# Optimization experiments

Hardware: AMD Instinct MI355X
Metric: run time of the kernel (lower is better)

## Reference

```python
import jax, jax.numpy as jnp
import numpy as np

B, N, C = 16, 1024, 768
NUM_HEADS = 8
HEAD_DIM = C // NUM_HEADS
TEMP_INIT = 0.05
EPS_NORM = 1e-12   # F.normalize eps
EPS_LN = 1e-5      # LayerNorm eps


def setup_inputs() -> dict:
    key = jax.random.key(0)
    ks = jax.random.split(key, 4)
    x = jax.random.normal(ks[0], (B, N, C), dtype=jnp.float32)
    w_qkv = jax.random.normal(ks[1], (3 * C, C), dtype=jnp.float32) * (1.0 / np.sqrt(C))
    w_proj = jax.random.normal(ks[2], (C, C), dtype=jnp.float32) * (1.0 / np.sqrt(C))
    temperature = jnp.ones((NUM_HEADS, 1, 1), dtype=jnp.float32) * TEMP_INIT
    conv_w = jax.random.normal(ks[3], (C, 1, 3, 3), dtype=jnp.float32) * (1.0 / 3.0)
    gamma = jnp.ones((C,), dtype=jnp.float32)
    beta = jnp.zeros((C,), dtype=jnp.float32)
    return {"x": x, "w_qkv": w_qkv, "w_proj": w_proj, "temperature": temperature,
            "conv_w": conv_w, "gamma": gamma, "beta": beta, "H": 32, "W": 32}


def _l2norm_tokens(t):
    # normalize along token dim (axis=-2), matching F.normalize(dim=-2)
    n = jnp.sqrt(jnp.sum(t * t, axis=-2, keepdims=True))
    return t / jnp.maximum(n, EPS_NORM)


def reference(x, w_qkv, w_proj, temperature, conv_w, gamma, beta, H, W):
    b, n, c = x.shape
    h, d = NUM_HEADS, HEAD_DIM
    qkv = (x @ w_qkv.T).reshape(b, n, 3, h, d).transpose(2, 0, 3, 1, 4)  # [3,B,h,N,d]
    q, k, v = qkv[0], qkv[1], qkv[2]
    q = _l2norm_tokens(q)
    k = _l2norm_tokens(k)
    # cross-covariance attention over channels: [B,h,d,d]
    A = jnp.einsum('bhnd,bhne->bhde', q, k) / temperature[None]
    A = jax.nn.softmax(A, axis=-1)
    # v @ A^T : [B,h,N,d]
    x_xca = jnp.einsum('bhne,bhde->bhnd', v, A)
    x_xca = x_xca.transpose(0, 2, 1, 3).reshape(b, n, c)
    x_xca = x_xca @ w_proj.T
    # depthwise 3x3 local propagation
    x_img = x.transpose(0, 2, 1).reshape(b, c, H, W)
    x_local = jax.lax.conv_general_dilated(
        x_img, conv_w, window_strides=(1, 1), padding=((1, 1), (1, 1)),
        dimension_numbers=('NCHW', 'OIHW', 'NCHW'), feature_group_count=c)
    x_local = x_local.reshape(b, c, n).transpose(0, 2, 1)
    y = x_xca + 0.1 * x_local
    mu = jnp.mean(y, axis=-1, keepdims=True)
    var = jnp.mean((y - mu) ** 2, axis=-1, keepdims=True)
    return (y - mu) * jax.lax.rsqrt(var + EPS_LN) * gamma + beta
```

## Files before the change

kernel.cpp:

```cpp
#include <hip/hip_runtime.h>

#define DEVI __device__ __forceinline__

typedef __bf16 bf16x8 __attribute__((ext_vector_type(8)));
typedef float f32x4 __attribute__((ext_vector_type(4)));

DEVI unsigned short f2bf(float f) {
  unsigned u = __builtin_bit_cast(unsigned, f);
  u += 0x7FFFu + ((u >> 16) & 1u);
  return (unsigned short)(u >> 16);
}
DEVI float bf2f(unsigned short s) {
  return __builtin_bit_cast(float, ((unsigned)s) << 16);
}
DEVI f32x4 mfma16(bf16x8 a, bf16x8 b, f32x4 c) {
  return __builtin_amdgcn_mfma_f32_16x16x32_bf16(a, b, c, 0, 0, 0);
}
DEVI void gload16(const void* g, void* l) {
  __builtin_amdgcn_global_load_lds(
      (const __attribute__((address_space(1))) void*)g,
      (__attribute__((address_space(3))) void*)l, 16, 0, 0);
}
template <int ROWB>
DEVI bf16x8 frag_ld(const char* lds, int row, int kb) {
  int off = row * ROWB + (kb ^ ((row & 7) << 4));
  return __builtin_bit_cast(bf16x8, *(const uint4*)(lds + off));
}

__global__ __launch_bounds__(256) void k_cvt2(const float* __restrict__ a,
                                              unsigned short* __restrict__ oa, int n4a,
                                              const float* __restrict__ b,
                                              unsigned short* __restrict__ ob, int n4b) {
  int i = blockIdx.x * 256 + threadIdx.x;
  int st = gridDim.x * 256;
  for (; i < n4a + n4b; i += st) {
    const float4* src = (i < n4a) ? ((const float4*)a) + i : ((const float4*)b) + (i - n4a);
    unsigned short* dst = (i < n4a) ? oa + 4 * (size_t)i : ob + 4 * (size_t)(i - n4a);
    float4 f = *src;
    ushort4 o;
    o.x = f2bf(f.x); o.y = f2bf(f.y); o.z = f2bf(f.z); o.w = f2bf(f.w);
    *(ushort4*)dst = o;
  }
}

template <int MODE>
__global__ __launch_bounds__(512, 4) void k_gemm(const unsigned short* __restrict__ A,
                                                 const unsigned short* __restrict__ B0,
                                                 unsigned short* __restrict__ o0,
                                                 unsigned short* __restrict__ o1,
                                                 unsigned short* __restrict__ o2) {
  __shared__ alignas(16) char lds[81920];
  const int tid = threadIdx.x, l = tid & 63, wid = tid >> 6;
  const int wr = wid >> 2, wc = wid & 3;
  const int xg = blockIdx.x;
  const int CPX = MODE ? 64 : 192;
  const int NJT = MODE ? 4 : 12;
  const int li = (xg & 7) * CPX + (xg >> 3);
  const int jt = li % NJT, mt = li / NJT;
  const int m0 = mt * 128, j0 = jt * 192;
  const unsigned short* Bb = MODE ? B0 + (size_t)(m0 >> 10) * 589824 : B0;

  const unsigned short* srcg[4][2];
  int ldso[4][2];
#pragma unroll
  for (int sg = 0; sg < 4; ++sg) {
    const bool isA = (sg == 0) || (sg == 3);
#pragma unroll
    for (int i = 0; i < 2; ++i) {
      int c;
      if (sg == 0)      c = (wid < 4) ? wid : wid + 4;
      else if (sg == 3) c = (wid < 4) ? wid + 4 : wid + 8;
      else if (sg == 1) { int cc = 2 * wid + i; c = (cc >> 2) * 6 + (cc & 3); }
      else              c = (wid >> 1) * 6 + 4 + (wid & 1);
      const int r0 = 8 * c;
      const int r = r0 + (l >> 3);
      const int scol = ((l & 7) ^ (l >> 3)) << 3;
      srcg[sg][i] = (isA ? A + (size_t)(m0 + r) * 768 : Bb + (size_t)(j0 + r) * 768) + scol;
      ldso[sg][i] = (isA ? 0 : 16384) + r0 * 128;
    }
  }
  const int swz = (l & 7) << 4;
  const int uu = (l >> 4) << 4;
  const int c0 = uu ^ swz;
  const int c1 = (64 | uu) ^ swz;
  const int arow = (wr * 64 + (l & 15)) * 128;
  const int brow = 16384 + (wc * 48 + (l & 15)) * 128;

  f32x4 acc[4][3];
#pragma unroll
  for (int i = 0; i < 4; ++i)
#pragma unroll
    for (int j = 0; j < 3; ++j)
#pragma unroll
      for (int e = 0; e < 4; ++e) acc[i][j][e] = 0.f;
  bf16x8 a[2][2], b01[2][2], b2[2];

#define STAGE1(sg, nxt, ko) \
  gload16(srcg[sg][0] + (ko), lds + (nxt)*40960 + ldso[sg][0])
#define STAGE2(sg, nxt, ko)                                        \
  do {                                                             \
    gload16(srcg[sg][0] + (ko), lds + (nxt)*40960 + ldso[sg][0]);  \
    gload16(srcg[sg][1] + (ko), lds + (nxt)*40960 + ldso[sg][1]);  \
  } while (0)
#define LD128(off) __builtin_bit_cast(bf16x8, *(const uint4*)(cb_ + (off)))

  STAGE1(0, 0, 0); STAGE2(1, 0, 0); STAGE1(2, 0, 0); STAGE1(3, 0, 0);
  asm volatile("s_waitcnt vmcnt(2)" ::: "memory");
  __builtin_amdgcn_s_barrier();

#define KBODY(KT, LASTF)                                                              \
  {                                                                                   \
    const char* cb_ = lds + ((KT) & 1) * 40960;                                       \
    const int nxt = (((KT) & 1) ^ 1);                                                 \
    const int ko = ((KT) + 1) * 64;                                                   \
    _Pragma("unroll") for (int mf = 0; mf < 2; ++mf) {                                \
      a[mf][0] = LD128(arow + mf * 2048 + c0);                                        \
      a[mf][1] = LD128(arow + mf * 2048 + c1);                                        \
    }                                                                                 \
    _Pragma("unroll") for (int nf = 0; nf < 2; ++nf) {                                \
      b01[nf][0] = LD128(brow + nf * 2048 + c0);                                      \
      b01[nf][1] = LD128(brow + nf * 2048 + c1);                                      \
    }                                                                                 \
    if (!(LASTF)) { STAGE1(0, nxt, ko); asm volatile("s_waitcnt vmcnt(2)" ::: "memory"); } \
    else          { asm volatile("s_waitcnt vmcnt(1)" ::: "memory"); }                \
    __builtin_amdgcn_s_barrier();                                                     \
    __builtin_amdgcn_s_setprio(1);                                                    \
    _Pragma("unroll") for (int mf = 0; mf < 2; ++mf)                                  \
      _Pragma("unroll") for (int nf = 0; nf < 2; ++nf) {                              \
        acc[mf][nf] = mfma16(a[mf][0], b01[nf][0], acc[mf][nf]);                      \
        acc[mf][nf] = mfma16(a[mf][1], b01[nf][1], acc[mf][nf]);                      \
      }                                                                               \
    __builtin_amdgcn_s_setprio(0);                                                    \
    b2[0] = LD128(brow + 2 * 2048 + c0);                                              \
    b2[1] = LD128(brow + 2 * 2048 + c1);                                              \
    if (!(LASTF)) { STAGE2(1, nxt, ko); asm volatile("s_waitcnt vmcnt(3)" ::: "memory"); } \
    else          { asm volatile("s_waitcnt vmcnt(0)" ::: "memory"); }                \
    __builtin_amdgcn_s_barrier();                                                     \
    __builtin_amdgcn_s_setprio(1);                                                    \
    _Pragma("unroll") for (int mf = 0; mf < 2; ++mf) {                                \
      acc[mf][2] = mfma16(a[mf][0], b2[0], acc[mf][2]);                               \
      acc[mf][2] = mfma16(a[mf][1], b2[1], acc[mf][2]);                               \
    }                                                                                 \
    __builtin_amdgcn_s_setprio(0);                                                    \
    _Pragma("unroll") for (int mf = 0; mf < 2; ++mf) {                                \
      a[mf][0] = LD128(arow + (mf + 2) * 2048 + c0);                                  \
      a[mf][1] = LD128(arow + (mf + 2) * 2048 + c1);                                  \
    }                                                                                 \
    if (!(LASTF)) STAGE1(2, nxt, ko);                                                 \
    asm volatile("" ::: "memory");                                                    \
    __builtin_amdgcn_s_barrier();                                                     \
    __builtin_amdgcn_s_setprio(1);                                                    \
    _Pragma("unroll") for (int mf = 0; mf < 2; ++mf)                                  \
      _Pragma("unroll") for (int nf = 0; nf < 2; ++nf) {                              \
        acc[mf + 2][nf] = mfma16(a[mf][0], b01[nf][0], acc[mf + 2][nf]);              \
        acc[mf + 2][nf] = mfma16(a[mf][1], b01[nf][1], acc[mf + 2][nf]);              \
      }                                                                               \
    __builtin_amdgcn_s_setprio(0);                                                    \
    if (!(LASTF)) { STAGE1(3, nxt, ko); asm volatile("s_waitcnt vmcnt(2)" ::: "memory"); } \
    else          { asm volatile("" ::: "memory"); }                                  \
    __builtin_amdgcn_s_barrier();                                                     \
    __builtin_amdgcn_s_setprio(1);                                                    \
    _Pragma("unroll") for (int mf = 0; mf < 2; ++mf) {                                \
      acc[mf + 2][2] = mfma16(a[mf][0], b2[0], acc[mf + 2][2]);                       \
      acc[mf + 2][2] = mfma16(a[mf][1], b2[1], acc[mf + 2][2]);                       \
    }                                                                                 \
    __builtin_amdgcn_s_setprio(0);                                                    \
  }

#pragma unroll 1
  for (int kt = 0; kt < 11; ++kt) KBODY(kt, false);
  KBODY(11, true);
#undef KBODY
#undef STAGE2
#undef STAGE1
#undef LD128

  if constexpr (MODE == 0) {
    const int s = j0 / 768;
    const int jin0 = (j0 % 768) + wc * 48 + (l & 15);
    const int ntok0 = m0 + wr * 64 + ((l >> 4) << 2);
#pragma unroll
    for (int mf = 0; mf < 4; ++mf) {
      const int nt = ntok0 + mf * 16;
      const int bb = nt >> 10, nin = nt & 1023;
#pragma unroll
      for (int nf = 0; nf < 3; ++nf) {
        const int jj = jin0 + nf * 16;
        const int hh = jj / 96, dd = jj % 96;
        if (s == 2) {
          unsigned short* vp = o2 + (size_t)nt * 768 + jj;
#pragma unroll
          for (int rr = 0; rr < 4; ++rr) vp[rr * 768] = f2bf(acc[mf][nf][rr]);
        } else {
          unsigned short* base = (s == 0) ? o0 : o1;
          ushort4 pk;
          pk.x = f2bf(acc[mf][nf][0]); pk.y = f2bf(acc[mf][nf][1]);
          pk.z = f2bf(acc[mf][nf][2]); pk.w = f2bf(acc[mf][nf][3]);
          *(ushort4*)(base + ((size_t)((bb * 8 + hh) * 96 + dd)) * 1024 + nin) = pk;
        }
      }
    }
  } else {
    const int ntok0 = m0 + wr * 64 + ((l >> 4) << 2);
    const int col0 = j0 + wc * 48 + (l & 15);
#pragma unroll
    for (int mf = 0; mf < 4; ++mf)
#pragma unroll
      for (int nf = 0; nf < 3; ++nf) {
        unsigned short* yp = o0 + (size_t)(ntok0 + mf * 16) * 768 + col0 + nf * 16;
#pragma unroll
        for (int rr = 0; rr < 4; ++rr) yp[rr * 768] = f2bf(acc[mf][nf][rr]);
      }
  }
}

DEVI float ssq8(uint4 u) {
  unsigned a[4] = {u.x, u.y, u.z, u.w};
  float s = 0.f;
#pragma unroll
  for (int i = 0; i < 4; ++i) {
    float lo = __builtin_bit_cast(float, a[i] << 16);
    float hi = __builtin_bit_cast(float, a[i] & 0xFFFF0000u);
    s += lo * lo + hi * hi;
  }
  return s;
}

__global__ __launch_bounds__(256) void k_attn(const unsigned short* __restrict__ qT,
                                              const unsigned short* __restrict__ kT,
                                              const float* __restrict__ temp,
                                              unsigned short* __restrict__ PT) {
  __shared__ alignas(16) char lQK[2][24576];
  __shared__ float lA[96 * 96];
  __shared__ float lrq[96], lrk[96];
  const int bh = blockIdx.x, tid = threadIdx.x, lane = tid & 63, wid = tid >> 6;
  const float invt = 1.f / temp[bh & 7];
  const int wr = wid >> 1, wc = wid & 1;
  const unsigned short* qb = qT + (size_t)bh * 96 * 1024;
  const unsigned short* kb = kT + (size_t)bh * 96 * 1024;

  const unsigned short* srcp[6];
  int dsto[6];
#pragma unroll
  for (int i = 0; i < 6; ++i) {
    int cid = wid * 6 + i;
    bool isK = cid >= 12;
    int c = isK ? cid - 12 : cid;
    int p = c * 1024 + lane * 16;
    int r = p >> 7, cb = p & 127;
    int cbs = cb ^ ((r & 7) << 4);
    srcp[i] = (isK ? kb : qb) + (size_t)r * 1024 + (cbs >> 1);
    dsto[i] = (isK ? 12288 : 0) + c * 1024;
  }

#pragma unroll
  for (int i = 0; i < 6; ++i) gload16(srcp[i], lQK[0] + dsto[i]);

  for (int row = wid; row < 192; row += 4) {
    const unsigned short* src = (row < 96) ? qb + (size_t)row * 1024
                                           : kb + (size_t)(row - 96) * 1024;
    const uint4* p = (const uint4*)src + lane * 2;
    float s = ssq8(p[0]) + ssq8(p[1]);
#pragma unroll
    for (int off = 32; off; off >>= 1) s += __shfl_xor(s, off, 64);
    if (lane == 0) {
      float r = 1.f / fmaxf(sqrtf(s), 1e-12f);
      if (row < 96) lrq[row] = r;
      else          lrk[row - 96] = r;
    }
  }

  f32x4 acc[3][3];
#pragma unroll
  for (int i = 0; i < 3; ++i)
#pragma unroll
    for (int j = 0; j < 3; ++j)
#pragma unroll
      for (int e = 0; e < 4; ++e) acc[i][j][e] = 0.f;

  asm volatile("s_waitcnt vmcnt(0)" ::: "memory");
  __builtin_amdgcn_s_barrier();

#pragma unroll 1
  for (int kt = 0; kt < 16; ++kt) {
    const char* bq = lQK[kt & 1];
    if (kt < 15) {
      char* nb = lQK[(kt + 1) & 1];
      const int ko = (kt + 1) * 64;
#pragma unroll
      for (int i = 0; i < 6; ++i) gload16(srcp[i] + ko, nb + dsto[i]);
    }
#pragma unroll
    for (int ks = 0; ks < 2; ++ks) {
      const int kb2 = ks * 64 + ((lane >> 4) << 4);
      bf16x8 af[3], bfv[3];
#pragma unroll
      for (int mb = 0; mb < 3; ++mb) af[mb] = frag_ld<128>(bq, wr * 48 + mb * 16 + (lane & 15), kb2);
#pragma unroll
      for (int nb2 = 0; nb2 < 3; ++nb2) bfv[nb2] = frag_ld<128>(bq + 12288, wc * 48 + nb2 * 16 + (lane & 15), kb2);
#pragma unroll
      for (int mb = 0; mb < 3; ++mb)
#pragma unroll
        for (int nb2 = 0; nb2 < 3; ++nb2) acc[mb][nb2] = mfma16(af[mb], bfv[nb2], acc[mb][nb2]);
    }
    asm volatile("s_waitcnt vmcnt(0)" ::: "memory");
    __builtin_amdgcn_s_barrier();
  }

  const int rb = wr * 48 + ((lane >> 4) << 2);
  const int eb = wc * 48 + (lane & 15);
#pragma unroll
  for (int mb = 0; mb < 3; ++mb)
#pragma unroll
    for (int nb = 0; nb < 3; ++nb) {
      int e = eb + nb * 16;
#pragma unroll
      for (int rr = 0; rr < 4; ++rr) {
        int d = rb + mb * 16 + rr;
        lA[d * 96 + e] = acc[mb][nb][rr] * lrq[d] * lrk[e] * invt;
      }
    }
  __syncthreads();
  for (int d = wid; d < 96; d += 4) {
    float v0 = lA[d * 96 + lane];
    float v1 = (lane < 32) ? lA[d * 96 + 64 + lane] : -3.0e38f;
    float mx = fmaxf(v0, v1);
#pragma unroll
    for (int off = 32; off; off >>= 1) mx = fmaxf(mx, __shfl_xor(mx, off, 64));
    float p0 = __expf(v0 - mx);
    float p1 = (lane < 32) ? __expf(v1 - mx) : 0.f;
    float ssum = p0 + p1;
#pragma unroll
    for (int off = 32; off; off >>= 1) ssum += __shfl_xor(ssum, off, 64);
    float rs = 1.f / ssum;
    PT[((size_t)bh * 96 + lane) * 96 + d] = f2bf(p0 * rs);
    if (lane < 32) PT[((size_t)bh * 96 + 64 + lane) * 96 + d] = f2bf(p1 * rs);
  }
}

__global__ __launch_bounds__(256) void k_prep(const unsigned short* __restrict__ PT,
                                              const float* __restrict__ wproj,
                                              unsigned short* __restrict__ B_all) {
  __shared__ alignas(16) char pl[19968 + 39936];
  unsigned short* lPt = (unsigned short*)pl;
  unsigned short* lW  = (unsigned short*)(pl + 19968);
  unsigned short* tr  = lW;
  const int blk = blockIdx.x;
  const int b = blk >> 5, h = (blk >> 2) & 7, cq = blk & 3;
  const int tid = threadIdx.x, l = tid & 63, wid = tid >> 6;
  const int wr = wid >> 1, wc = wid & 1;

  const unsigned short* pt = PT + (size_t)(b * 8 + h) * 96 * 96;
  for (int idx = tid; idx < 1152; idx += 256) {
    int r = idx / 12, ch = idx % 12;
    *(uint4*)(lPt + r * 104 + ch * 8) = *(const uint4*)(pt + r * 96 + ch * 8);
  }
  for (int idx = tid; idx < 4608; idx += 256) {
    int r = idx / 24, ch = idx % 24;
    float4 f = *(const float4*)(wproj + (size_t)(cq * 192 + r) * 768 + h * 96 + ch * 4);
    ushort4 o;
    o.x = f2bf(f.x); o.y = f2bf(f.y); o.z = f2bf(f.z); o.w = f2bf(f.w);
    *(ushort4*)(lW + r * 104 + ch * 4) = o;
  }
  __syncthreads();

  f32x4 acc[3][6];
#pragma unroll
  for (int i = 0; i < 3; ++i)
#pragma unroll
    for (int j = 0; j < 6; ++j)
#pragma unroll
      for (int e = 0; e < 4; ++e) acc[i][j][e] = 0.f;

#pragma unroll
  for (int ks = 0; ks < 3; ++ks) {
    const int kof = ks * 32 + ((l >> 4) << 3);
    bf16x8 af[3], bv[6];
#pragma unroll
    for (int mb = 0; mb < 3; ++mb)
      af[mb] = __builtin_bit_cast(bf16x8, *(const uint4*)(lPt + (wr * 48 + mb * 16 + (l & 15)) * 104 + kof));
#pragma unroll
    for (int nb = 0; nb < 6; ++nb)
      bv[nb] = __builtin_bit_cast(bf16x8, *(const uint4*)(lW + (wc * 96 + nb * 16 + (l & 15)) * 104 + kof));
#pragma unroll
    for (int mb = 0; mb < 3; ++mb)
#pragma unroll
      for (int nb = 0; nb < 6; ++nb) acc[mb][nb] = mfma16(af[mb], bv[nb], acc[mb][nb]);
  }

  __syncthreads();
  const int e0 = wr * 48 + ((l >> 4) << 2);
  const int cl0 = wc * 96 + (l & 15);
#pragma unroll
  for (int mb = 0; mb < 3; ++mb)
#pragma unroll
    for (int nb = 0; nb < 6; ++nb) {
      ushort4 pk;
      pk.x = f2bf(acc[mb][nb][0]); pk.y = f2bf(acc[mb][nb][1]);
      pk.z = f2bf(acc[mb][nb][2]); pk.w = f2bf(acc[mb][nb][3]);
      *(ushort4*)(tr + (cl0 + nb * 16) * 100 + e0 + mb * 16) = pk;
    }
  __syncthreads();
  for (int idx = tid; idx < 2304; idx += 256) {
    int r = idx / 12, ch = idx % 12;
    uint4 u = *(const uint4*)(tr + r * 100 + ch * 8);
    *(uint4*)(B_all + ((size_t)(b * 768) + cq * 192 + r) * 768 + h * 96 + ch * 8) = u;
  }
}

__global__ __launch_bounds__(256) void k_final(const unsigned short* __restrict__ yp,
                                               const unsigned short* __restrict__ xb16,
                                               const float* __restrict__ cw,
                                               const float* __restrict__ gamma,
                                               const float* __restrict__ beta,
                                               float* __restrict__ out) {
  const int wid = threadIdx.x >> 6, lane = threadIdx.x & 63;
  const int m = blockIdx.x * 4 + wid;
  const int bb = m >> 10, n = m & 1023, yy = n >> 5, xx = n & 31;
  const unsigned short* xb = xb16 + (size_t)bb * 1024 * 768;

  float yv[3][4];
#pragma unroll
  for (int g = 0; g < 3; ++g) {
    const int c = g * 256 + lane * 4;
    float w36[36];
    const float4* wp = (const float4*)(cw + (size_t)c * 9);
#pragma unroll
    for (int i = 0; i < 9; ++i) *(float4*)(w36 + i * 4) = wp[i];

    float a0 = 0.f, a1 = 0.f, a2 = 0.f, a3 = 0.f;
#pragma unroll
    for (int dy = -1; dy <= 1; ++dy) {
      int ny = yy + dy;
      if ((unsigned)ny < 32u) {
#pragma unroll
        for (int dx = -1; dx <= 1; ++dx) {
          int nx = xx + dx;
          if ((unsigned)nx < 32u) {
            ushort4 v = *(const ushort4*)(xb + (size_t)(ny * 32 + nx) * 768 + c);
            const int j = (dy + 1) * 3 + (dx + 1);
            a0 += w36[0 * 9 + j] * bf2f(v.x);
            a1 += w36[1 * 9 + j] * bf2f(v.y);
            a2 += w36[2 * 9 + j] * bf2f(v.z);
            a3 += w36[3 * 9 + j] * bf2f(v.w);
          }
        }
      }
    }
    ushort4 f = *(const ushort4*)(yp + (size_t)m * 768 + c);
    yv[g][0] = bf2f(f.x) + 0.1f * a0;
    yv[g][1] = bf2f(f.y) + 0.1f * a1;
    yv[g][2] = bf2f(f.z) + 0.1f * a2;
    yv[g][3] = bf2f(f.w) + 0.1f * a3;
  }

  float s1 = 0.f, s2 = 0.f;
#pragma unroll
  for (int g = 0; g < 3; ++g)
#pragma unroll
    for (int e = 0; e < 4; ++e) { s1 += yv[g][e]; s2 += yv[g][e] * yv[g][e]; }
#pragma unroll
  for (int off = 32; off; off >>= 1) {
    s1 += __shfl_xor(s1, off, 64);
    s2 += __shfl_xor(s2, off, 64);
  }
  const float mu = s1 * (1.f / 768.f);
  const float var = s2 * (1.f / 768.f) - mu * mu;
  const float rs = rsqrtf(var + 1e-5f);

#pragma unroll
  for (int g = 0; g < 3; ++g) {
    const int c = g * 256 + lane * 4;
    float4 gm = *(const float4*)(gamma + c);
    float4 bt = *(const float4*)(beta + c);
    float4 o;
    o.x = (yv[g][0] - mu) * rs * gm.x + bt.x;
    o.y = (yv[g][1] - mu) * rs * gm.y + bt.y;
    o.z = (yv[g][2] - mu) * rs * gm.z + bt.z;
    o.w = (yv[g][3] - mu) * rs * gm.w + bt.w;
    *(float4*)(out + (size_t)m * 768 + c) = o;
  }
}

extern "C" void kernel_launch(void* const* d_in, const int* in_sizes, int n_in,
                              void* d_out, int out_size, void* d_ws, size_t ws_size,
                              hipStream_t stream) {
  const float* x     = (const float*)d_in[0];
  const float* wqkv  = (const float*)d_in[1];
  const float* wproj = (const float*)d_in[2];
  const float* temp  = (const float*)d_in[3];
  const float* cw    = (const float*)d_in[4];
  const float* gamma = (const float*)d_in[5];
  const float* beta  = (const float*)d_in[6];
  float* out = (float*)d_out;
  char* ws = (char*)d_ws;

  unsigned short* xb    = (unsigned short*)(ws);
  unsigned short* wqb   = (unsigned short*)(ws + 25165824);
  unsigned short* qT    = (unsigned short*)(ws + 28704768);
  unsigned short* yp    = qT;
  unsigned short* kT    = (unsigned short*)(ws + 53870592);
  unsigned short* B_all = kT;
  unsigned short* vP    = (unsigned short*)(ws + 79036416);
  unsigned short* PT    = (unsigned short*)(ws + 104202240);

  k_cvt2<<<dim3(2048), dim3(256), 0, stream>>>(x, xb, 16384 * 768 / 4,
                                               wqkv, wqb, 2304 * 768 / 4);
  k_gemm<0><<<dim3(1536), dim3(512), 0, stream>>>(xb, wqb, qT, kT, vP);
  k_attn<<<dim3(128), dim3(256), 0, stream>>>(qT, kT, temp, PT);
  k_prep<<<dim3(512), dim3(256), 0, stream>>>(PT, wproj, B_all);
  k_gemm<1><<<dim3(512), dim3(512), 0, stream>>>(vP, B_all, yp, nullptr, nullptr);
  k_final<<<dim3(4096), dim3(256), 0, stream>>>(yp, xb, cw, gamma, beta, out);
}
```

Baseline: 229.9 us.

## Restructure GEMM k-loop into two barrier phases with separate A-fragment registers

The GEMM main loop goes from four barrier-separated MFMA phases to two. A second A-fragment register set (a2) is added so the lower-half A rows can be loaded from LDS early, and global-to-LDS prefetches are issued in two larger batches. The convert kernel also gives x and w_qkv fixed, branch-free block ranges instead of a per-element select. The aim is fewer barriers and waitcnt stalls per k-step, paid for with more registers, which may lower occupancy under the 512x4 launch bound.

```diff
diff --git a/kernel.cpp b/kernel.cpp
--- a/kernel.cpp
+++ b/kernel.cpp
@@ -31,25 +31,29 @@
                                               unsigned short* __restrict__ oa, int n4a,
                                               const float* __restrict__ b,
                                               unsigned short* __restrict__ ob, int n4b) {
-  int i = blockIdx.x * 256 + threadIdx.x;
-  int st = gridDim.x * 256;
-  for (; i < n4a + n4b; i += st) {
-    const float4* src = (i < n4a) ? ((const float4*)a) + i : ((const float4*)b) + (i - n4a);
-    unsigned short* dst = (i < n4a) ? oa + 4 * (size_t)i : ob + 4 * (size_t)(i - n4a);
-    float4 f = *src;
-    ushort4 o;
-    o.x = f2bf(f.x); o.y = f2bf(f.y); o.z = f2bf(f.z); o.w = f2bf(f.w);
-    *(ushort4*)dst = o;
+  const int tid = threadIdx.x;
+  if (blockIdx.x < 1792) {
+    for (int i = blockIdx.x * 256 + tid; i < n4a; i += 1792 * 256) {
+      float4 f = ((const float4*)a)[i];
+      ushort4 o;
+      o.x = f2bf(f.x); o.y = f2bf(f.y); o.z = f2bf(f.z); o.w = f2bf(f.w);
+      ((ushort4*)oa)[i] = o;
+    }
+  } else {
+    for (int i = (blockIdx.x - 1792) * 256 + tid; i < n4b; i += 256 * 256) {
+      float4 f = ((const float4*)b)[i];
+      ushort4 o;
+      o.x = f2bf(f.x); o.y = f2bf(f.y); o.z = f2bf(f.z); o.w = f2bf(f.w);
+      ((ushort4*)ob)[i] = o;
+    }
   }
 }
 
 template <int MODE>
-__global__ __launch_bounds__(512, 4) void k_gemm(const unsigned short* __restrict__ A,
-                                                 const unsigned short* __restrict__ B0,
-                                                 unsigned short* __restrict__ o0,
-                                                 unsigned short* __restrict__ o1,
-                                                 unsigned short* __restrict__ o2) {
-  __shared__ alignas(16) char lds[81920];
+DEVI void gemm_body(char* lds, const unsigned short* __restrict__ A,
+                    const unsigned short* __restrict__ B0,
+                    unsigned short* __restrict__ o0, unsigned short* __restrict__ o1,
+                    unsigned short* __restrict__ o2) {
   const int tid = threadIdx.x, l = tid & 63, wid = tid >> 6;
   const int wr = wid >> 2, wc = wid & 3;
   const int xg = blockIdx.x;
@@ -93,7 +97,7 @@
     for (int j = 0; j < 3; ++j)
 #pragma unroll
       for (int e = 0; e < 4; ++e) acc[i][j][e] = 0.f;
-  bf16x8 a[2][2], b01[2][2], b2[2];
+  bf16x8 a[2][2], a2[2][2], b01[2][2], b2[2];
 
 #define STAGE1(sg, nxt, ko) \
   gload16(srcg[sg][0] + (ko), lds + (nxt)*40960 + ldso[sg][0])
@@ -113,6 +117,7 @@
     const char* cb_ = lds + ((KT) & 1) * 40960;                                       \
     const int nxt = (((KT) & 1) ^ 1);                                                 \
     const int ko = ((KT) + 1) * 64;                                                   \
+                           \
     _Pragma("unroll") for (int mf = 0; mf < 2; ++mf) {                                \
       a[mf][0] = LD128(arow + mf * 2048 + c0);                                        \
       a[mf][1] = LD128(arow + mf * 2048 + c1);                                        \
@@ -121,8 +126,12 @@
       b01[nf][0] = LD128(brow + nf * 2048 + c0);                                      \
       b01[nf][1] = LD128(brow + nf * 2048 + c1);                                      \
     }                                                                                 \
-    if (!(LASTF)) { STAGE1(0, nxt, ko); asm volatile("s_waitcnt vmcnt(2)" ::: "memory"); } \
-    else          { asm volatile("s_waitcnt vmcnt(1)" ::: "memory"); }                \
+    if (!(LASTF)) {                                                                   \
+      STAGE1(0, nxt, ko); STAGE2(1, nxt, ko);                                         \
+      asm volatile("s_waitcnt vmcnt(3)" ::: "memory");                                \
+    } else {                                                                          \
+      asm volatile("s_waitcnt vmcnt(0)" ::: "memory");                                \
+    }                                                                                 \
     __builtin_amdgcn_s_barrier();                                                     \
     __builtin_amdgcn_s_setprio(1);                                                    \
     _Pragma("unroll") for (int mf = 0; mf < 2; ++mf)                                  \
@@ -131,38 +140,31 @@
         acc[mf][nf] = mfma16(a[mf][1], b01[nf][1], acc[mf][nf]);                      \
       }                                                                               \
     __builtin_amdgcn_s_setprio(0);                                                    \
+              \
     b2[0] = LD128(brow + 2 * 2048 + c0);                                              \
     b2[1] = LD128(brow + 2 * 2048 + c1);                                              \
-    if (!(LASTF)) { STAGE2(1, nxt, ko); asm volatile("s_waitcnt vmcnt(3)" ::: "memory"); } \
-    else          { asm volatile("s_waitcnt vmcnt(0)" ::: "memory"); }                \
+    _Pragma("unroll") for (int mf = 0; mf < 2; ++mf) {                                \
+      a2[mf][0] = LD128(arow + (mf + 2) * 2048 + c0);                                 \
+      a2[mf][1] = LD128(arow + (mf + 2) * 2048 + c1);                                 \
+    }                                                                                 \
+    if (!(LASTF)) {                                                                   \
+      STAGE1(2, nxt, ko); STAGE1(3, nxt, ko);                                         \
+      asm volatile("s_waitcnt vmcnt(2)" ::: "memory");                                \
+    }                                                                                 \
     __builtin_amdgcn_s_barrier();                                                     \
     __builtin_amdgcn_s_setprio(1);                                                    \
     _Pragma("unroll") for (int mf = 0; mf < 2; ++mf) {                                \
       acc[mf][2] = mfma16(a[mf][0], b2[0], acc[mf][2]);                               \
       acc[mf][2] = mfma16(a[mf][1], b2[1], acc[mf][2]);                               \
     }                                                                                 \
-    __builtin_amdgcn_s_setprio(0);                                                    \
-    _Pragma("unroll") for (int mf = 0; mf < 2; ++mf) {                                \
-      a[mf][0] = LD128(arow + (mf + 2) * 2048 + c0);                                  \
-      a[mf][1] = LD128(arow + (mf + 2) * 2048 + c1);                                  \
-    }                                                                                 \
-    if (!(LASTF)) STAGE1(2, nxt, ko);                                                 \
-    asm volatile("" ::: "memory");                                                    \
-    __builtin_amdgcn_s_barrier();                                                     \
-    __builtin_amdgcn_s_setprio(1);                                                    \
     _Pragma("unroll") for (int mf = 0; mf < 2; ++mf)                                  \
       _Pragma("unroll") for (int nf = 0; nf < 2; ++nf) {                              \
-        acc[mf + 2][nf] = mfma16(a[mf][0], b01[nf][0], acc[mf + 2][nf]);              \
-        acc[mf + 2][nf] = mfma16(a[mf][1], b01[nf][1], acc[mf + 2][nf]);              \
+        acc[mf + 2][nf] = mfma16(a2[mf][0], b01[nf][0], acc[mf + 2][nf]);             \
+        acc[mf + 2][nf] = mfma16(a2[mf][1], b01[nf][1], acc[mf + 2][nf]);             \
       }                                                                               \
-    __builtin_amdgcn_s_setprio(0);                                                    \
-    if (!(LASTF)) { STAGE1(3, nxt, ko); asm volatile("s_waitcnt vmcnt(2)" ::: "memory"); } \
-    else          { asm volatile("" ::: "memory"); }                                  \
-    __builtin_amdgcn_s_barrier();                                                     \
-    __builtin_amdgcn_s_setprio(1);                                                    \
     _Pragma("unroll") for (int mf = 0; mf < 2; ++mf) {                                \
-      acc[mf + 2][2] = mfma16(a[mf][0], b2[0], acc[mf + 2][2]);                       \
-      acc[mf + 2][2] = mfma16(a[mf][1], b2[1], acc[mf + 2][2]);                       \
+      acc[mf + 2][2] = mfma16(a2[mf][0], b2[0], acc[mf + 2][2]);                      \
+      acc[mf + 2][2] = mfma16(a2[mf][1], b2[1], acc[mf + 2][2]);                      \
     }                                                                                 \
     __builtin_amdgcn_s_setprio(0);                                                    \
   }
@@ -212,6 +214,21 @@
         for (int rr = 0; rr < 4; ++rr) yp[rr * 768] = f2bf(acc[mf][nf][rr]);
       }
   }
+}
+
+__global__ __launch_bounds__(512, 4) void kg0_qkv(const unsigned short* __restrict__ A,
+                                                  const unsigned short* __restrict__ B0,
+                                                  unsigned short* __restrict__ o0,
+                                                  unsigned short* __restrict__ o1,
+                                                  unsigned short* __restrict__ o2) {
+  __shared__ alignas(16) char lds[81920];
+  gemm_body<0>(lds, A, B0, o0, o1, o2);
+}
+__global__ __launch_bounds__(512, 4) void kg1_proj(const unsigned short* __restrict__ A,
+                                                   const unsigned short* __restrict__ B0,
+                                                   unsigned short* __restrict__ o0) {
+  __shared__ alignas(16) char lds[81920];
+  gemm_body<1>(lds, A, B0, o0, nullptr, nullptr);
 }
 
 DEVI float ssq8(uint4 u) {
@@ -506,9 +523,9 @@
 
   k_cvt2<<<dim3(2048), dim3(256), 0, stream>>>(x, xb, 16384 * 768 / 4,
                                                wqkv, wqb, 2304 * 768 / 4);
-  k_gemm<0><<<dim3(1536), dim3(512), 0, stream>>>(xb, wqb, qT, kT, vP);
+  kg0_qkv<<<dim3(1536), dim3(512), 0, stream>>>(xb, wqb, qT, kT, vP);
   k_attn<<<dim3(128), dim3(256), 0, stream>>>(qT, kT, temp, PT);
   k_prep<<<dim3(512), dim3(256), 0, stream>>>(PT, wproj, B_all);
-  k_gemm<1><<<dim3(512), dim3(512), 0, stream>>>(vP, B_all, yp, nullptr, nullptr);
+  kg1_proj<<<dim3(512), dim3(512), 0, stream>>>(vP, B_all, yp);
   k_final<<<dim3(4096), dim3(256), 0, stream>>>(yp, xb, cw, gamma, beta, out);
 }
```

After: 230.5 us. Within noise of the previous version (+0.3%).
